# Performance work log

Hardware: AMD Instinct MI355X
Metric: run time of the kernel (lower is better)

## Reference

```python
import jax, jax.numpy as jnp
import numpy as np

B, D, N = 8, 512, 4096
K = 2048  # codebook_size


def setup_inputs() -> dict:
    key = jax.random.key(0)
    k1, k2 = jax.random.split(key)
    x = jax.random.normal(k1, (B, D, N), dtype=jnp.float32)
    embed = jax.random.normal(k2, (K, D), dtype=jnp.float32)
    return {"x": x, "embed": embed}


def reference(x, embed):
    # x: [b, d, n] -> [b, n, d] (project_in is Identity since codebook_dim == dim)
    xt = jnp.transpose(x, (0, 2, 1))  # [b, n, d]
    # squared euclidean distances (argmin-equivalent to torch.cdist argmin)
    x2 = jnp.sum(xt * xt, axis=-1, keepdims=True)          # [b, n, 1]
    e2 = jnp.sum(embed * embed, axis=-1)                   # [k]
    cross = jnp.einsum("bnd,kd->bnk", xt, embed)           # [b, n, k]
    dist = x2 - 2.0 * cross + e2                           # [b, n, k]
    embed_ind = jnp.argmin(dist, axis=-1)                  # [b, n] int
    quantize = embed[embed_ind]                            # [b, n, d] gather
    # project_out Identity, then rearrange 'b n d -> b d n'
    quantize = jnp.transpose(quantize, (0, 2, 1))          # [b, d, n]
    return quantize, embed_ind
```

## Files before the change

kernel.cpp:

```cpp
#include <hip/hip_runtime.h>
#include <math.h>

#define DDIM 512
#define NNN  4096
#define KKK  2048
#define MMM  32768

#define TMQ  128
#define TNC  256
#define BK   32
#define KSPLIT 2
#define KHALF (KKK/KSPLIT)
#define NKT  (KHALF/TNC)
#define NDR  (DDIM/BK)
#define TOTR (NKT*NDR)
#define BUFS ((TMQ+TNC)*BK)
#define TAU  0.25f
#define CAPF 4096

#define XH_OFF   0
#define EH_OFF   8388608
#define PART_OFF (EH_OFF + 524288)
#define XF_OFF   (PART_OFF + MMM*KSPLIT*4)
#define KEY_OFF  (XF_OFF + 2097152)
#define LIST_OFF (KEY_OFF + 8192)
#define CNT_OFF  (LIST_OFF + CAPF)
#define IDX_OFF  ((size_t)MMM * DDIM)

typedef short short8v __attribute__((ext_vector_type(8)));
typedef float f32x4   __attribute__((ext_vector_type(4)));

__device__ inline unsigned short f2bf(float f) {
  unsigned u = __float_as_uint(f);
  u = u + 0x7FFFu + ((u >> 16) & 1u);
  return (unsigned short)(u >> 16);
}

__device__ inline void gl_lds16(const short* g, short* l) {
  __builtin_amdgcn_global_load_lds(
      (const __attribute__((address_space(1))) unsigned int*)g,
      (__attribute__((address_space(3))) unsigned int*)l, 16, 0, 0);
}

__device__ inline unsigned mono(float f) {
  unsigned u = __float_as_uint(f);
  return (u & 0x80000000u) ? ~u : (u | 0x80000000u);
}

__global__ void conv_e(const float* __restrict__ embed, float* __restrict__ halfe2,
                       float* __restrict__ out) {
  const int gid = blockIdx.x * 256 + threadIdx.x;
  if (gid == 0) *(int*)&out[CNT_OFF] = 0;
  if (gid < CAPF) ((unsigned long long*)&out[KEY_OFF])[gid] = ~0ull;
  const int row  = blockIdx.x * 4 + (threadIdx.x >> 6);
  const int lane = threadIdx.x & 63;
  const float* e = embed + (size_t)row * DDIM;
  short* eh = (short*)&out[EH_OFF];
  const float4 v0 = *(const float4*)&e[lane*8];
  const float4 v1 = *(const float4*)&e[lane*8 + 4];
  const float vv[8] = {v0.x,v0.y,v0.z,v0.w,v1.x,v1.y,v1.z,v1.w};
  float s = 0.f;
  short8v p;
  #pragma unroll
  for (int i = 0; i < 8; ++i) { s = fmaf(vv[i], vv[i], s); p[i] = (short)f2bf(vv[i]); }
  *(short8v*)&eh[(size_t)row * DDIM + lane*8] = p;
  #pragma unroll
  for (int off = 32; off >= 1; off >>= 1) s += __shfl_xor(s, off, 64);
  if (lane == 0) halfe2[row] = 0.5f * s;
}

__global__ __launch_bounds__(256)
void conv_x(const float* __restrict__ x, float* __restrict__ out) {
  __shared__ float xt[64][65];
  const int t  = threadIdx.x;
  const int nt = blockIdx.x & 63, dt = (blockIdx.x >> 6) & 7, b = blockIdx.x >> 9;
  const int n0 = nt * 64, d0 = dt * 64;
  const float* xb = x + ((size_t)b * DDIM + d0) * NNN + n0;
  #pragma unroll
  for (int i = 0; i < 4; ++i) {
    const int fid = t + 256*i;
    const int dl = fid >> 4, n4 = (fid & 15) * 4;
    const float4 v = *(const float4*)&xb[(size_t)dl * NNN + n4];
    xt[dl][n4+0] = v.x; xt[dl][n4+1] = v.y; xt[dl][n4+2] = v.z; xt[dl][n4+3] = v.w;
  }
  __syncthreads();
  short* xh = (short*)&out[XH_OFF];
  const int m0 = b * NNN + n0;
  #pragma unroll
  for (int i = 0; i < 2; ++i) {
    const int id = t + 256*i;
    const int m = id >> 3, ch = (id & 7) * 8;
    short8v p;
    #pragma unroll
    for (int j = 0; j < 8; ++j) p[j] = (short)f2bf(xt[ch + j][m]);
    *(short8v*)&xh[(size_t)(m0 + m) * DDIM + d0 + ch] = p;
  }
}

__global__ __launch_bounds__(256, 2)
void vq_main(const float* __restrict__ halfe2, float* __restrict__ out) {
  __shared__ __align__(16) short lds[2 * BUFS];
  const short* xh = (const short*)&out[XH_OFF];
  const short* eh = (const short*)&out[EH_OFF];

  const int t  = threadIdx.x;
  const int mb = blockIdx.x >> 1, ks = blockIdx.x & 1;
  const int q0 = mb * TMQ;
  const int kbase = ks * KHALF;
  const int w = t >> 6, lane = t & 63;
  const int mw = (w >> 1) * 64, nw = (w & 1) * 128;
  const int l15 = lane & 15, lg = lane >> 4;
  const int c0 = w * 6;
  const int lrow = lane >> 2;
  const int scol = ((((lane & 3) - ((lane >> 3) & 3)) & 3) << 3);

  float rv1[16], rv2[16]; int ri1[16];
  #pragma unroll
  for (int i = 0; i < 16; ++i) { rv1[i] = INFINITY; rv2[i] = INFINITY; ri1[i] = 0x7FFFFFFF; }

  auto STAGE = [&](int R) {
    const int kt = R >> 4, dr = R & 15;
    const int kb_ = kbase + kt * TNC;
    const int d0 = dr * BK;
    short* buf = lds + (R & 1) * BUFS;
    #pragma unroll
    for (int j = 0; j < 6; ++j) {
      const int c = c0 + j;
      const short* src = (c < 8)
        ? xh + (size_t)(q0 + c*16 + lrow) * DDIM + d0 + scol
        : eh + (size_t)(kb_ + (c-8)*16 + lrow) * DDIM + d0 + scol;
      gl_lds16(src, buf + c * 512);
    }
  };

  STAGE(0);
  asm volatile("s_waitcnt vmcnt(0)" ::: "memory");
  __builtin_amdgcn_s_barrier();

  for (int kt = 0; kt < NKT; ++kt) {
    const int kb = kbase + kt * TNC;
    f32x4 acc[4][8];
    #pragma unroll
    for (int mi = 0; mi < 4; ++mi)
      #pragma unroll
      for (int ni = 0; ni < 8; ++ni) acc[mi][ni] = (f32x4){0.f,0.f,0.f,0.f};

    #pragma unroll 2
    for (int dr = 0; dr < NDR; ++dr) {
      const int R = kt * NDR + dr;
      const short* cur = lds + (R & 1) * BUFS;
      if (R + 1 < TOTR) STAGE(R + 1);
      const short* xs = cur;
      const short* es = cur + TMQ * BK;
      short8v bfr[8];
      #pragma unroll
      for (int ni = 0; ni < 8; ++ni) {
        const int row = nw + ni*16 + l15;
        bfr[ni] = *(const short8v*)&es[row*32 + (((lg + (row >> 1)) & 3) << 3)];
      }
      #pragma unroll
      for (int mi = 0; mi < 4; ++mi) {
        const int row = mw + mi*16 + l15;
        const short8v a = *(const short8v*)&xs[row*32 + (((lg + (row >> 1)) & 3) << 3)];
        #pragma unroll
        for (int ni = 0; ni < 8; ++ni)
          acc[mi][ni] = __builtin_amdgcn_mfma_f32_16x16x32_bf16(a, bfr[ni], acc[mi][ni], 0,0,0);
      }
      asm volatile("s_waitcnt vmcnt(0)" ::: "memory");
      __builtin_amdgcn_s_barrier();
    }

    float he[8];
    #pragma unroll
    for (int ni = 0; ni < 8; ++ni) he[ni] = halfe2[kb + nw + ni*16 + l15];
    #pragma unroll
    for (int mi = 0; mi < 4; ++mi) {
      #pragma unroll
      for (int r = 0; r < 4; ++r) {
        const int e_ = mi*4 + r;
        #pragma unroll
        for (int ni = 0; ni < 8; ++ni) {
          const float sc = he[ni] - acc[mi][ni][r];
          if (sc < rv1[e_]) { rv2[e_] = rv1[e_]; rv1[e_] = sc; ri1[e_] = kb + nw + ni*16 + l15; }
          else rv2[e_] = fminf(rv2[e_], sc);
        }
      }
    }
  }

  #pragma unroll
  for (int e_ = 0; e_ < 16; ++e_) {
    float v1 = rv1[e_], v2 = rv2[e_]; int i1 = ri1[e_];
    #pragma unroll
    for (int off = 1; off < 16; off <<= 1) {
      const float ov1 = __shfl_xor(v1, off, 64);
      const int   oi1 = __shfl_xor(i1, off, 64);
      const float ov2 = __shfl_xor(v2, off, 64);
      if (ov1 < v1 || (ov1 == v1 && oi1 < i1)) { v2 = fminf(v1, ov2); v1 = ov1; i1 = oi1; }
      else v2 = fminf(v2, ov1);
    }
    rv1[e_] = v1; rv2[e_] = v2; ri1[e_] = i1;
  }

  __syncthreads();
  float* mbuf = (float*)lds;
  if (l15 == 0) {
    #pragma unroll
    for (int mi = 0; mi < 4; ++mi)
      #pragma unroll
      for (int r = 0; r < 4; ++r) {
        const int ql = mw + mi*16 + lg*4 + r;
        const int slot = (ql*2 + (w & 1))*3;
        const int e_ = mi*4 + r;
        mbuf[slot+0] = rv1[e_];
        mbuf[slot+1] = __int_as_float(ri1[e_]);
        mbuf[slot+2] = rv2[e_];
      }
  }
  __syncthreads();
  if (t < TMQ) {
    const float a1 = mbuf[t*6+0]; const int ai = __float_as_int(mbuf[t*6+1]); const float a2 = mbuf[t*6+2];
    const float b1 = mbuf[t*6+3]; const int bi = __float_as_int(mbuf[t*6+4]); const float b2 = mbuf[t*6+5];
    float v1, v2; int i1;
    if (b1 < a1 || (b1 == a1 && bi < ai)) { v1 = b1; i1 = bi; v2 = fminf(a1, b2); }
    else                                  { v1 = a1; i1 = ai; v2 = fminf(a2, b1); }
    f32x4 st = {v1, (float)i1, v2, 0.f};
    *(f32x4*)&out[PART_OFF + ((size_t)(q0 + t)*KSPLIT + ks)*4] = st;
  }
}

__global__ void vq_merge(float* __restrict__ out) {
  const int q = blockIdx.x * 256 + threadIdx.x;
  float v1, v2; int i1;
  {
    const f32x4 p = *(const f32x4*)&out[PART_OFF + (size_t)q*(KSPLIT*4)];
    v1 = p[0]; i1 = (int)p[1]; v2 = p[2];
  }
  #pragma unroll
  for (int s = 1; s < KSPLIT; ++s) {
    const f32x4 p = *(const f32x4*)&out[PART_OFF + (size_t)q*(KSPLIT*4) + s*4];
    const float b1 = p[0]; const int bi = (int)p[1]; const float b2 = p[2];
    if (b1 < v1 || (b1 == v1 && bi < i1)) { v2 = fminf(v1, b2); v1 = b1; i1 = bi; }
    else v2 = fminf(v2, b1);
  }
  out[IDX_OFF + q] = (float)i1;
  if (v2 - v1 < TAU) {
    const int pos = atomicAdd((int*)&out[CNT_OFF], 1);
    if (pos < CAPF) ((int*)&out[LIST_OFF])[pos] = q;
  }
}

__global__ __launch_bounds__(256)
void vq_prep(const float* __restrict__ x, float* __restrict__ out) {
  const int nf0 = *(const int*)&out[CNT_OFF];
  const int nf  = nf0 < CAPF ? nf0 : CAPF;
  const int* list = (const int*)&out[LIST_OFF];
  float* XF = &out[XF_OFF];
  const int wid  = (blockIdx.x * 256 + threadIdx.x) >> 6;
  const int lane = threadIdx.x & 63;
  for (int s = wid; s < nf; s += 1024) {
    const int q = list[s];
    const int b = q >> 12, n = q & (NNN - 1);
    const float* xb = x + (size_t)b * DDIM * NNN + n;
    #pragma unroll
    for (int j = 0; j < 8; ++j) {
      const int d = lane + 64*j;
      XF[(size_t)s * DDIM + d] = xb[(size_t)d * NNN];
    }
  }
}

__global__ __launch_bounds__(256, 2)
void vq_refine(const float* __restrict__ embed, const float* __restrict__ halfe2,
               float* __restrict__ out) {
  const int nf0 = *(const int*)&out[CNT_OFF];
  const int nf  = nf0 < CAPF ? nf0 : CAPF;
  const int s0  = blockIdx.y * 64;
  if (s0 >= nf) return;
  __shared__ float xs[32][68];
  __shared__ float es[32][132];
  const int t = threadIdx.x, tx = t & 15, ty = t >> 4;
  const int kb = blockIdx.x * 128;
  const float* XF = &out[XF_OFF];
  unsigned long long* keys = (unsigned long long*)&out[KEY_OFF];

  float acc[4][8];
  #pragma unroll
  for (int i = 0; i < 4; ++i)
    #pragma unroll
    for (int j = 0; j < 8; ++j) acc[i][j] = 0.f;

  for (int dc = 0; dc < 16; ++dc) {
    __syncthreads();
    #pragma unroll
    for (int i = 0; i < 2; ++i) {
      const int l = t + 256*i;
      const int m = l >> 3, f = l & 7;
      const float4 v = *(const float4*)&XF[(size_t)(s0 + m) * DDIM + dc*32 + 4*f];
      xs[4*f+0][m] = v.x; xs[4*f+1][m] = v.y; xs[4*f+2][m] = v.z; xs[4*f+3][m] = v.w;
    }
    #pragma unroll
    for (int i = 0; i < 4; ++i) {
      const int l = t + 256*i;
      const int k = l >> 3, f = l & 7;
      const float4 v = *(const float4*)&embed[(size_t)(kb + k)*DDIM + dc*32 + 4*f];
      es[4*f+0][k] = v.x; es[4*f+1][k] = v.y; es[4*f+2][k] = v.z; es[4*f+3][k] = v.w;
    }
    __syncthreads();
    #pragma unroll
    for (int d = 0; d < 32; ++d) {
      const float4 a4 = *(const float4*)&xs[d][ty*4];
      const float4 b0 = *(const float4*)&es[d][tx*4];
      const float4 b1 = *(const float4*)&es[d][64 + tx*4];
      const float a[4]  = {a4.x, a4.y, a4.z, a4.w};
      const float bb[8] = {b0.x, b0.y, b0.z, b0.w, b1.x, b1.y, b1.z, b1.w};
      #pragma unroll
      for (int i = 0; i < 4; ++i)
        #pragma unroll
        for (int j = 0; j < 8; ++j)
          acc[i][j] = fmaf(a[i], bb[j], acc[i][j]);
    }
  }

  const int kb0 = kb + tx*4, kb1 = kb + 64 + tx*4;
  const float4 h0 = *(const float4*)&halfe2[kb0];
  const float4 h1 = *(const float4*)&halfe2[kb1];
  const float hh[8] = {h0.x, h0.y, h0.z, h0.w, h1.x, h1.y, h1.z, h1.w};
  #pragma unroll
  for (int i = 0; i < 4; ++i) {
    float v = hh[0] - acc[i][0];
    int  vi = kb0;
    #pragma unroll
    for (int j = 1; j < 8; ++j) {
      const float w  = hh[j] - acc[i][j];
      const int   wk = (j < 4) ? (kb0 + j) : (kb1 + j - 4);
      if (w < v) { v = w; vi = wk; }
    }
    #pragma unroll
    for (int off = 1; off < 16; off <<= 1) {
      const float ov = __shfl_xor(v, off, 64);
      const int   oi = __shfl_xor(vi, off, 64);
      if (ov < v || (ov == v && oi < vi)) { v = ov; vi = oi; }
    }
    if (tx == 0) {
      const unsigned long long key =
          ((unsigned long long)mono(v) << 32) | (unsigned)vi;
      atomicMin(&keys[s0 + ty*4 + i], key);
    }
  }
}

__global__ void vq_apply(float* __restrict__ out) {
  const int slot = blockIdx.x * 256 + threadIdx.x;
  const int nf0 = *(const int*)&out[CNT_OFF];
  const int nf  = nf0 < CAPF ? nf0 : CAPF;
  if (slot >= nf) return;
  const int q = ((const int*)&out[LIST_OFF])[slot];
  const unsigned long long k = ((const unsigned long long*)&out[KEY_OFF])[slot];
  if (k != ~0ull) out[IDX_OFF + q] = (float)(unsigned)(k & 0xFFFFFFFFull);
}

__global__ __launch_bounds__(256)
void vq_gather(const float* __restrict__ embed, float* __restrict__ out) {
  __shared__ int idx_s[128];
  const int t  = threadIdx.x;
  const int q0 = blockIdx.x * 128;
  const int b  = q0 >> 12, n0 = q0 & (NNN-1);
  if (t < 128) idx_s[t] = (int)out[IDX_OFF + q0 + t];
  __syncthreads();
  float* qb = out + (size_t)b * DDIM * NNN + n0;
  for (int j = 0; j < 64; ++j) {
    const int id = t + 256*j;
    const int d = id >> 5, n4 = (id & 31) * 4;
    float4 v;
    v.x = embed[(size_t)idx_s[n4+0]*DDIM + d];
    v.y = embed[(size_t)idx_s[n4+1]*DDIM + d];
    v.z = embed[(size_t)idx_s[n4+2]*DDIM + d];
    v.w = embed[(size_t)idx_s[n4+3]*DDIM + d];
    *(float4*)&qb[(size_t)d * NNN + n4] = v;
  }
}

extern "C" void kernel_launch(void* const* d_in, const int* in_sizes, int n_in,
                              void* d_out, int out_size, void* d_ws, size_t ws_size,
                              hipStream_t stream) {
  const float* x     = (const float*)d_in[0];
  const float* embed = (const float*)d_in[1];
  float* out    = (float*)d_out;
  float* halfe2 = (float*)d_ws;

  hipLaunchKernelGGL(conv_e,   dim3(KKK/4),   dim3(256), 0, stream, embed, halfe2, out);
  hipLaunchKernelGGL(conv_x,   dim3(4096),    dim3(256), 0, stream, x, out);
  hipLaunchKernelGGL(vq_main,  dim3((MMM/TMQ)*KSPLIT), dim3(256), 0, stream, halfe2, out);
  hipLaunchKernelGGL(vq_merge, dim3(MMM/256), dim3(256), 0, stream, out);
  hipLaunchKernelGGL(vq_prep,  dim3(256),     dim3(256), 0, stream, x, out);
  hipLaunchKernelGGL(vq_refine,dim3(16, CAPF/64), dim3(256), 0, stream, embed, halfe2, out);
  hipLaunchKernelGGL(vq_apply, dim3(CAPF/256),dim3(256), 0, stream, out);
  hipLaunchKernelGGL(vq_gather,dim3(MMM/128), dim3(256), 0, stream, embed, out);
}
```

Measured before the change: 327.6 us.

## Triple-buffer vq_main LDS staging and merge embed/x conversion kernels

Moves the main distance GEMM from double to triple LDS buffering. Loads are issued two stages ahead and the wait uses a partial vmcnt, so global-to-LDS copies overlap more with MFMA work. It also folds the embed conversion kernel into the x transpose/convert kernel as extra blocks, removing one launch. The costs are a larger LDS footprint per block, which may cut occupancy below 2 blocks/CU, and the dropped unroll pragma on the inner loop.

```diff
diff --git a/kernel.cpp b/kernel.cpp
--- a/kernel.cpp
+++ b/kernel.cpp
@@ -15,6 +15,7 @@
 #define NDR  (DDIM/BK)
 #define TOTR (NKT*NDR)
 #define BUFS ((TMQ+TNC)*BK)
+#define NBUF 3
 #define TAU  0.25f
 #define CAPF 4096
 
@@ -47,32 +48,35 @@
   return (u & 0x80000000u) ? ~u : (u | 0x80000000u);
 }
 
-__global__ void conv_e(const float* __restrict__ embed, float* __restrict__ halfe2,
-                       float* __restrict__ out) {
-  const int gid = blockIdx.x * 256 + threadIdx.x;
-  if (gid == 0) *(int*)&out[CNT_OFF] = 0;
-  if (gid < CAPF) ((unsigned long long*)&out[KEY_OFF])[gid] = ~0ull;
-  const int row  = blockIdx.x * 4 + (threadIdx.x >> 6);
-  const int lane = threadIdx.x & 63;
-  const float* e = embed + (size_t)row * DDIM;
-  short* eh = (short*)&out[EH_OFF];
-  const float4 v0 = *(const float4*)&e[lane*8];
-  const float4 v1 = *(const float4*)&e[lane*8 + 4];
-  const float vv[8] = {v0.x,v0.y,v0.z,v0.w,v1.x,v1.y,v1.z,v1.w};
-  float s = 0.f;
-  short8v p;
-  #pragma unroll
-  for (int i = 0; i < 8; ++i) { s = fmaf(vv[i], vv[i], s); p[i] = (short)f2bf(vv[i]); }
-  *(short8v*)&eh[(size_t)row * DDIM + lane*8] = p;
-  #pragma unroll
-  for (int off = 32; off >= 1; off >>= 1) s += __shfl_xor(s, off, 64);
-  if (lane == 0) halfe2[row] = 0.5f * s;
-}
-
 __global__ __launch_bounds__(256)
-void conv_x(const float* __restrict__ x, float* __restrict__ out) {
+void conv_xe(const float* __restrict__ x, const float* __restrict__ embed,
+             float* __restrict__ halfe2, float* __restrict__ out) {
   __shared__ float xt[64][65];
-  const int t  = threadIdx.x;
+  const int t = threadIdx.x;
+
+  if (blockIdx.x >= 4096) {
+    const int blk = blockIdx.x - 4096;
+    const int gid = blk * 256 + t;
+    if (gid == 0) *(int*)&out[CNT_OFF] = 0;
+    if (gid < CAPF) ((unsigned long long*)&out[KEY_OFF])[gid] = ~0ull;
+    const int row  = blk * 4 + (t >> 6);
+    const int lane = t & 63;
+    const float* e = embed + (size_t)row * DDIM;
+    short* eh = (short*)&out[EH_OFF];
+    const float4 v0 = *(const float4*)&e[lane*8];
+    const float4 v1 = *(const float4*)&e[lane*8 + 4];
+    const float vv[8] = {v0.x,v0.y,v0.z,v0.w,v1.x,v1.y,v1.z,v1.w};
+    float s = 0.f;
+    short8v p;
+    #pragma unroll
+    for (int i = 0; i < 8; ++i) { s = fmaf(vv[i], vv[i], s); p[i] = (short)f2bf(vv[i]); }
+    *(short8v*)&eh[(size_t)row * DDIM + lane*8] = p;
+    #pragma unroll
+    for (int off = 32; off >= 1; off >>= 1) s += __shfl_xor(s, off, 64);
+    if (lane == 0) halfe2[row] = 0.5f * s;
+    return;
+  }
+
   const int nt = blockIdx.x & 63, dt = (blockIdx.x >> 6) & 7, b = blockIdx.x >> 9;
   const int n0 = nt * 64, d0 = dt * 64;
   const float* xb = x + ((size_t)b * DDIM + d0) * NNN + n0;
@@ -99,7 +103,7 @@
 
 __global__ __launch_bounds__(256, 2)
 void vq_main(const float* __restrict__ halfe2, float* __restrict__ out) {
-  __shared__ __align__(16) short lds[2 * BUFS];
+  __shared__ __align__(16) short lds[NBUF * BUFS];
   const short* xh = (const short*)&out[XH_OFF];
   const short* eh = (const short*)&out[EH_OFF];
 
@@ -118,25 +122,27 @@
   #pragma unroll
   for (int i = 0; i < 16; ++i) { rv1[i] = INFINITY; rv2[i] = INFINITY; ri1[i] = 0x7FFFFFFF; }
 
-  auto STAGE = [&](int R) {
-    const int kt = R >> 4, dr = R & 15;
-    const int kb_ = kbase + kt * TNC;
-    const int d0 = dr * BK;
-    short* buf = lds + (R & 1) * BUFS;
+  auto STAGE = [&](int R, int tb) {
+    const int kt_ = R >> 4, dr_ = R & 15;
+    const int kb_ = kbase + kt_ * TNC;
+    const int d0_ = dr_ * BK;
+    short* buf = lds + tb * BUFS;
     #pragma unroll
     for (int j = 0; j < 6; ++j) {
       const int c = c0 + j;
       const short* src = (c < 8)
-        ? xh + (size_t)(q0 + c*16 + lrow) * DDIM + d0 + scol
-        : eh + (size_t)(kb_ + (c-8)*16 + lrow) * DDIM + d0 + scol;
+        ? xh + (size_t)(q0 + c*16 + lrow) * DDIM + d0_ + scol
+        : eh + (size_t)(kb_ + (c-8)*16 + lrow) * DDIM + d0_ + scol;
       gl_lds16(src, buf + c * 512);
     }
   };
 
-  STAGE(0);
-  asm volatile("s_waitcnt vmcnt(0)" ::: "memory");
+  STAGE(0, 0);
+  STAGE(1, 1);
+  asm volatile("s_waitcnt vmcnt(6)" ::: "memory");
   __builtin_amdgcn_s_barrier();
 
+  int bi = 0;
   for (int kt = 0; kt < NKT; ++kt) {
     const int kb = kbase + kt * TNC;
     f32x4 acc[4][8];
@@ -145,13 +151,12 @@
       #pragma unroll
       for (int ni = 0; ni < 8; ++ni) acc[mi][ni] = (f32x4){0.f,0.f,0.f,0.f};
 
-    #pragma unroll 2
     for (int dr = 0; dr < NDR; ++dr) {
       const int R = kt * NDR + dr;
-      const short* cur = lds + (R & 1) * BUFS;
-      if (R + 1 < TOTR) STAGE(R + 1);
-      const short* xs = cur;
-      const short* es = cur + TMQ * BK;
+      const int nb = bi ? bi - 1 : 2;
+      if (R + 2 < TOTR) STAGE(R + 2, nb);
+      const short* xs = lds + bi * BUFS;
+      const short* es = xs + TMQ * BK;
       short8v bfr[8];
       #pragma unroll
       for (int ni = 0; ni < 8; ++ni) {
@@ -166,8 +171,10 @@
         for (int ni = 0; ni < 8; ++ni)
           acc[mi][ni] = __builtin_amdgcn_mfma_f32_16x16x32_bf16(a, bfr[ni], acc[mi][ni], 0,0,0);
       }
-      asm volatile("s_waitcnt vmcnt(0)" ::: "memory");
+      if (R + 2 < TOTR) { asm volatile("s_waitcnt vmcnt(6)" ::: "memory"); }
+      else              { asm volatile("s_waitcnt vmcnt(0)" ::: "memory"); }
       __builtin_amdgcn_s_barrier();
+      bi = (bi == 2) ? 0 : bi + 1;
     }
 
     float he[8];
@@ -220,10 +227,10 @@
   __syncthreads();
   if (t < TMQ) {
     const float a1 = mbuf[t*6+0]; const int ai = __float_as_int(mbuf[t*6+1]); const float a2 = mbuf[t*6+2];
-    const float b1 = mbuf[t*6+3]; const int bi = __float_as_int(mbuf[t*6+4]); const float b2 = mbuf[t*6+5];
+    const float b1 = mbuf[t*6+3]; const int bi2 = __float_as_int(mbuf[t*6+4]); const float b2 = mbuf[t*6+5];
     float v1, v2; int i1;
-    if (b1 < a1 || (b1 == a1 && bi < ai)) { v1 = b1; i1 = bi; v2 = fminf(a1, b2); }
-    else                                  { v1 = a1; i1 = ai; v2 = fminf(a2, b1); }
+    if (b1 < a1 || (b1 == a1 && bi2 < ai)) { v1 = b1; i1 = bi2; v2 = fminf(a1, b2); }
+    else                                   { v1 = a1; i1 = ai;  v2 = fminf(a2, b1); }
     f32x4 st = {v1, (float)i1, v2, 0.f};
     *(f32x4*)&out[PART_OFF + ((size_t)(q0 + t)*KSPLIT + ks)*4] = st;
   }
@@ -389,8 +396,7 @@
   float* out    = (float*)d_out;
   float* halfe2 = (float*)d_ws;
 
-  hipLaunchKernelGGL(conv_e,   dim3(KKK/4),   dim3(256), 0, stream, embed, halfe2, out);
-  hipLaunchKernelGGL(conv_x,   dim3(4096),    dim3(256), 0, stream, x, out);
+  hipLaunchKernelGGL(conv_xe, dim3(4096 + KKK/4), dim3(256), 0, stream, x, embed, halfe2, out);
   hipLaunchKernelGGL(vq_main,  dim3((MMM/TMQ)*KSPLIT), dim3(256), 0, stream, halfe2, out);
   hipLaunchKernelGGL(vq_merge, dim3(MMM/256), dim3(256), 0, stream, out);
   hipLaunchKernelGGL(vq_prep,  dim3(256),     dim3(256), 0, stream, x, out);
```

After: 320.0 us. -2.3%, faster.
